# Optimization experiments

Measured on AMD Instinct MI355X. Metric: run time of the kernel, lower is better.

Reference implementation:

```python
import jax, jax.numpy as jnp
import numpy as np

N, E, M, F, L = 50000, 800000, 50000, 64, 20
HID = 32
NEG_SLOPE = 0.2


def gatv2(x, src, dst, Wl, Wr, att, b, heads, outc):
    # PyG GATv2Conv (eval mode, dropout off), self-loops already in src/dst.
    n = x.shape[0]
    xl = (x @ Wl).reshape(n, heads, outc)
    xr = (x @ Wr).reshape(n, heads, outc)
    e = jax.nn.leaky_relu(xl[src] + xr[dst], NEG_SLOPE)          # [E, H, C]
    score = jnp.einsum('ehc,hc->eh', e, att)                      # [E, H]
    smax = jax.ops.segment_max(score, dst, num_segments=n)
    ex = jnp.exp(score - smax[dst])
    denom = jax.ops.segment_sum(ex, dst, num_segments=n)
    alpha = ex / denom[dst]                                       # scatter-softmax
    out = jax.ops.segment_sum(alpha[:, :, None] * xl[src], dst, num_segments=n)
    return out.reshape(n, heads * outc) + b


def setup_inputs() -> dict:
    key = jax.random.key(0)
    ks = jax.random.split(key, 32)
    d = {}
    d['x'] = jax.random.normal(ks[0], (N, 60), jnp.float32)
    d['lane_x'] = jax.random.normal(ks[1], (M, 2), jnp.float32)
    d['centerline'] = jax.random.normal(ks[2], (F, L, 2), jnp.float32)
    d['edge_index'] = jax.random.randint(ks[3], (2, E), 0, N)
    d['focal_idx'] = jax.random.randint(ks[4], (F,), 0, N)
    s = 0.1
    d['emb_W'] = jax.random.normal(ks[5], (60, HID)) * s
    d['emb_b'] = jnp.zeros((HID,))
    d['c1_Wl'] = jax.random.normal(ks[6], (HID, 4 * HID)) * s
    d['c1_Wr'] = jax.random.normal(ks[7], (HID, 4 * HID)) * s
    d['c1_att'] = jax.random.normal(ks[8], (4, HID)) * s
    d['c1_b'] = jnp.zeros((4 * HID,))
    d['c2_Wl'] = jax.random.normal(ks[9], (4 * HID, 4 * HID)) * s
    d['c2_Wr'] = jax.random.normal(ks[10], (4 * HID, 4 * HID)) * s
    d['c2_att'] = jax.random.normal(ks[11], (4, HID)) * s
    d['c2_b'] = jnp.zeros((4 * HID,))
    d['map_W'] = jax.random.normal(ks[12], (2, HID)) * s
    d['map_b'] = jnp.zeros((HID,))
    d['gg_Wl'] = jax.random.normal(ks[13], (4 * HID, HID)) * s
    d['gg_Wr'] = jax.random.normal(ks[14], (4 * HID, HID)) * s
    d['gg_att'] = jax.random.normal(ks[15], (1, HID)) * s
    d['gg_b'] = jnp.zeros((HID,))
    d['cl_W'] = jax.random.normal(ks[16], (2, HID)) * s
    d['cl_b'] = jnp.zeros((HID,))
    d['fc1_W'] = jax.random.normal(ks[17], (3 * HID, HID)) * s
    d['fc1_b'] = jnp.zeros((HID,))
    d['fc2_W'] = jax.random.normal(ks[18], (HID, HID // 2)) * s
    d['fc2_b'] = jnp.zeros((HID // 2,))
    d['fco_W'] = jax.random.normal(ks[19], (HID // 2, 60)) * s
    d['fco_b'] = jnp.zeros((60,))
    return d


def reference(x, lane_x, centerline, edge_index, focal_idx,
              emb_W, emb_b, c1_Wl, c1_Wr, c1_att, c1_b,
              c2_Wl, c2_Wr, c2_att, c2_b, map_W, map_b,
              gg_Wl, gg_Wr, gg_att, gg_b, cl_W, cl_b,
              fc1_W, fc1_b, fc2_W, fc2_b, fco_W, fco_b):
    n = x.shape[0]
    loops = jnp.arange(n)
    src = jnp.concatenate([edge_index[0], loops])  # PyG adds self-loops
    dst = jnp.concatenate([edge_index[1], loops])
    # agent encoder + subgraph (two GATv2 layers, heads=4, concat)
    h = jax.nn.relu(x @ emb_W + emb_b)                                   # [N,32]
    h = jax.nn.relu(gatv2(h, src, dst, c1_Wl, c1_Wr, c1_att, c1_b, 4, HID))
    agent_feat = jax.nn.relu(gatv2(h, src, dst, c2_Wl, c2_Wr, c2_att, c2_b, 4, HID))  # [N,128]
    # map branch (executable path: no lane edges -> plain embedding + mean pool)
    map_x = jax.nn.relu(lane_x @ map_W + map_b)                          # [M,32]
    map_global = jnp.mean(map_x, axis=0, keepdims=True)                  # [1,32]
    # global graph (heads=1)
    gf = jax.nn.relu(gatv2(agent_feat, src, dst, gg_Wl, gg_Wr, gg_att, gg_b, 1, HID))  # [N,32]
    focal = gf[focal_idx]                                                # [F,32]
    map_g = jnp.broadcast_to(map_global, (focal.shape[0], HID))
    cl = jnp.mean(centerline, axis=1) @ cl_W + cl_b                      # [F,32]
    comb = jnp.concatenate([focal, map_g, cl], axis=1)                   # [F,96]
    h = jax.nn.relu(comb @ fc1_W + fc1_b)
    h = jax.nn.relu(h @ fc2_W + fc2_b)
    return h @ fco_W + fco_b                                             # [F,60]
```

## Files before the change

kernel.cpp:

```cpp
#include <hip/hip_runtime.h>
#include <hip/hip_bf16.h>
#include <hip/hip_fp16.h>

typedef _Float16 half_t;
typedef _Float16 h8 __attribute__((ext_vector_type(8)));
typedef _Float16 h4v __attribute__((ext_vector_type(4)));
typedef _Float16 h2v __attribute__((ext_vector_type(2)));
typedef float f4v __attribute__((ext_vector_type(4)));

union H8u { h8 v; h2v h2[4]; _Float16 e[8]; };
union H4u { h4v v; h2v h2[2]; _Float16 e[4]; };

static inline int cdiv(long a, long b) { return (int)((a + b - 1) / b); }

__device__ __forceinline__ void fma4(float4& a, float s, const float4& w) {
    a.x += s * w.x; a.y += s * w.y; a.z += s * w.z; a.w += s * w.w;
}

__device__ __forceinline__ h8 hmax8(h8 a, h8 b) {
#if __has_builtin(__builtin_elementwise_max)
    return __builtin_elementwise_max(a, b);
#else
    h8 r;
#pragma unroll
    for (int j = 0; j < 8; ++j) r[j] = (a[j] > b[j]) ? a[j] : b[j];
    return r;
#endif
}
__device__ __forceinline__ h4v hmax4(h4v a, h4v b) {
#if __has_builtin(__builtin_elementwise_max)
    return __builtin_elementwise_max(a, b);
#else
    h4v r;
#pragma unroll
    for (int j = 0; j < 4; ++j) r[j] = (a[j] > b[j]) ? a[j] : b[j];
    return r;
#endif
}

__device__ __forceinline__ float dot2acc(h2v a, h2v b, float c) {
#if __has_builtin(__builtin_amdgcn_fdot2)
    return __builtin_amdgcn_fdot2(a, b, c, false);
#else
    return c + (float)a.x * (float)b.x + (float)a.y * (float)b.y;
#endif
}


template <int K4, int C4, int R>
__global__ __launch_bounds__(256) void gemm_t_h(
        const float* __restrict__ X, const float* __restrict__ W,
        const float* __restrict__ bias, half_t* __restrict__ Y,
        int Nr, int relu) {
    int idx = blockIdx.x * blockDim.x + threadIdx.x;
    int total = (Nr / R) * C4;
    if (idx >= total) return;
    int c4 = idx % C4;
    int n0 = (idx / C4) * R;
    const float4* __restrict__ Wv = (const float4*)W;
    const float4* __restrict__ Xv = (const float4*)X;
    float4 acc[R];
    float4 binit = bias ? ((const float4*)bias)[c4] : make_float4(0.f, 0.f, 0.f, 0.f);
#pragma unroll
    for (int r = 0; r < R; ++r) acc[r] = binit;
#pragma unroll 4
    for (int k4 = 0; k4 < K4; ++k4) {
        float4 w0 = Wv[(size_t)(4 * k4 + 0) * C4 + c4];
        float4 w1 = Wv[(size_t)(4 * k4 + 1) * C4 + c4];
        float4 w2 = Wv[(size_t)(4 * k4 + 2) * C4 + c4];
        float4 w3 = Wv[(size_t)(4 * k4 + 3) * C4 + c4];
#pragma unroll
        for (int r = 0; r < R; ++r) {
            float4 xv = Xv[(size_t)(n0 + r) * K4 + k4];
            fma4(acc[r], xv.x, w0); fma4(acc[r], xv.y, w1);
            fma4(acc[r], xv.z, w2); fma4(acc[r], xv.w, w3);
        }
    }
#pragma unroll
    for (int r = 0; r < R; ++r) {
        float4 o = acc[r];
        if (relu) {
            o.x = fmaxf(o.x, 0.f); o.y = fmaxf(o.y, 0.f);
            o.z = fmaxf(o.z, 0.f); o.w = fmaxf(o.w, 0.f);
        }
        h4v oh; oh.x = (half_t)o.x; oh.y = (half_t)o.y; oh.z = (half_t)o.z; oh.w = (half_t)o.w;
        ((h4v*)Y)[(size_t)(n0 + r) * C4 + c4] = oh;
    }
}


__global__ void wtrans(const float* __restrict__ c1l, const float* __restrict__ c1r,
                       const float* __restrict__ c2l, const float* __restrict__ c2r,
                       const float* __restrict__ ggl, const float* __restrict__ ggr,
                       const float* __restrict__ at1, const float* __restrict__ at2,
                       const float* __restrict__ atg, half_t* __restrict__ dst) {
    int idx = blockIdx.x * blockDim.x + threadIdx.x;
    if (idx >= 49440) return;
    if (idx >= 49152) {
        int j = idx - 49152;
        float v = (j < 128) ? at1[j] : (j < 256) ? at2[j - 128] : atg[j - 256];
        dst[idx] = (half_t)v;
        return;
    }
    const float* src; int K, loc;
    if (idx < 8192) {
        K = 32;
        if (idx < 4096) { src = c1l; loc = idx; } else { src = c1r; loc = idx - 4096; }
        int k = loc % K, c = loc / K;
        dst[idx] = (half_t)src[k * 128 + c];
    } else if (idx < 40960) {
        K = 128;
        if (idx < 24576) { src = c2l; loc = idx - 8192; } else { src = c2r; loc = idx - 24576; }
        int k = loc % K, c = loc / K;
        dst[idx] = (half_t)src[k * 128 + c];
    } else {
        K = 128;
        if (idx < 45056) { src = ggl; loc = idx - 40960; } else { src = ggr; loc = idx - 45056; }
        int k = loc % K, c = loc / K;
        dst[idx] = (half_t)src[k * 32 + c];
    }
}


template <int K, int C1>
__global__ __launch_bounds__(256) void mfma_dual(
        const half_t* __restrict__ Xh,
        const half_t* __restrict__ W1t, const half_t* __restrict__ W2t,
        half_t* __restrict__ Y1, half_t* __restrict__ Y2, int Nr) {
    constexpr int KT = K / 32;
    constexpr int NBC = (2 * C1) / 64;
    int wave = threadIdx.x >> 6, lane = threadIdx.x & 63;
    int bCol = blockIdx.x % NBC;
    int bRow = blockIdx.x / NBC;
    int rowBase = bRow * 128 + wave * 32;
    int colBase = bCol * 64;
    int m = lane & 15, quad = lane >> 4;

    f4v acc[2][4] = {};

    const half_t* bptr[4];
#pragma unroll
    for (int nt = 0; nt < 4; ++nt) {
        int gc = colBase + nt * 16 + m;
        bptr[nt] = (gc < C1) ? (W1t + (size_t)gc * K) : (W2t + (size_t)(gc - C1) * K);
    }
    int r0 = rowBase + m, r1 = rowBase + 16 + m;
    int r0c = (r0 < Nr) ? r0 : (Nr - 1);
    int r1c = (r1 < Nr) ? r1 : (Nr - 1);
    const half_t* a0p = Xh + (size_t)r0c * K + quad * 8;
    const half_t* a1p = Xh + (size_t)r1c * K + quad * 8;

#pragma unroll
    for (int kk = 0; kk < KT; ++kk) {
        h8 a0 = *(const h8*)(a0p + kk * 32);
        h8 a1 = *(const h8*)(a1p + kk * 32);
#pragma unroll
        for (int nt = 0; nt < 4; ++nt) {
            h8 b = *(const h8*)(bptr[nt] + kk * 32 + quad * 8);
            acc[0][nt] = __builtin_amdgcn_mfma_f32_16x16x32_f16(a0, b, acc[0][nt], 0, 0, 0);
            acc[1][nt] = __builtin_amdgcn_mfma_f32_16x16x32_f16(a1, b, acc[1][nt], 0, 0, 0);
        }
    }

#pragma unroll
    for (int mt = 0; mt < 2; ++mt) {
#pragma unroll
        for (int nt = 0; nt < 4; ++nt) {
            int gc = colBase + nt * 16 + m;
            half_t* Y = (gc < C1) ? (Y1 + gc) : (Y2 + (gc - C1));
#pragma unroll
            for (int r = 0; r < 4; ++r) {
                int gr = rowBase + mt * 16 + quad * 4 + r;
                if (gr < Nr) Y[(size_t)gr * C1] = (half_t)acc[mt][nt][r];
            }
        }
    }
}


__global__ void count_dst(const int* __restrict__ ei, int* __restrict__ counts, int E) {
    int e = blockIdx.x * blockDim.x + threadIdx.x;
    if (e >= E) return;
    atomicAdd(&counts[ei[E + e]], 1);
}

#define SCAN_CH 2048

__global__ void reduce_chunks(const int* __restrict__ counts, int* __restrict__ partial, int N) {
    __shared__ int sh[256];
    int t = threadIdx.x, base = blockIdx.x * SCAN_CH + t * 8;
    int s = 0;
    for (int j = 0; j < 8; ++j) if (base + j < N) s += counts[base + j] + 1;
    sh[t] = s; __syncthreads();
    for (int off = 128; off >= 1; off >>= 1) {
        if (t < off) sh[t] += sh[t + off];
        __syncthreads();
    }
    if (t == 0) partial[blockIdx.x] = sh[0];
}

__global__ void scan_partials(int* __restrict__ partial, int nch) {
    if (threadIdx.x == 0 && blockIdx.x == 0) {
        int run = 0;
        for (int i = 0; i < nch; ++i) { int v = partial[i]; partial[i] = run; run += v; }
    }
}

__global__ void scan_chunks(int* __restrict__ counts, const int* __restrict__ partial,
                            int* __restrict__ offsets, int* __restrict__ cursor,
                            int* __restrict__ adj, int N) {
    __shared__ int sh[256];
    int t = threadIdx.x, b = blockIdx.x, base = b * SCAN_CH + t * 8;
    int v[8], s = 0;
    for (int j = 0; j < 8; ++j) {
        v[j] = (base + j < N) ? (counts[base + j] + 1) : 0;
        s += v[j];
    }
    sh[t] = s; __syncthreads();
    for (int off = 1; off < 256; off <<= 1) {
        int x = (t >= off) ? sh[t - off] : 0;
        __syncthreads();
        sh[t] += x;
        __syncthreads();
    }
    int run = partial[b] + (t == 0 ? 0 : sh[t - 1]);
    for (int j = 0; j < 8; ++j) {
        if (base + j < N) {
            offsets[base + j] = run;
            adj[run] = base + j;
            cursor[base + j] = run + 1;
            counts[base + j] = v[j];
        }
        run += v[j];
    }
}

__global__ __launch_bounds__(256) void fill_adj_sliced(
        const int* __restrict__ ei, int* __restrict__ cursor,
        int* __restrict__ adj, int E, int sliceSz) {
    int slice = blockIdx.x & 7;
    int lo = slice * sliceSz, hi = lo + sliceSz;
    int nb = gridDim.x >> 3;
    int bi = blockIdx.x >> 3;
    int stride = nb * 256;
    for (int e = bi * 256 + threadIdx.x; e < E; e += stride) {
        int d = ei[E + e];
        if (d >= lo && d < hi) {
            int pos = atomicAdd(&cursor[d], 1);
            adj[pos] = ei[e];
        }
    }
}


__global__ __launch_bounds__(256) void gat8_h4(
        const half_t* __restrict__ xl, const half_t* __restrict__ xr,
        const half_t* __restrict__ atth, const int* __restrict__ offsets,
        const int* __restrict__ counts, const int* __restrict__ adj,
        const float* __restrict__ bias, half_t* __restrict__ out, int N) {
    int wave = threadIdx.x >> 6, lane = threadIdx.x & 63;
    int g = lane >> 3, t = lane & 7;
    int d = blockIdx.x * 32 + wave * 8 + g;
    int dc = (d < N) ? d : (N - 1);
    int off = offsets[dc];
    int deg = (d < N) ? counts[dc] : 0;
    int dmax = deg;
    dmax = max(dmax, __shfl_xor(dmax, 8));
    dmax = max(dmax, __shfl_xor(dmax, 16));
    dmax = max(dmax, __shfl_xor(dmax, 32));

    const half_t* xrp = xr + (size_t)dc * 128 + t * 16;
    h8 xr_lo = *(const h8*)(xrp);
    h8 xr_hi = *(const h8*)(xrp + 8);
    H8u at_lo, at_hi;
    at_lo.v = *(const h8*)(atth + t * 16);
    at_hi.v = *(const h8*)(atth + t * 16 + 8);

    float acc[16];
#pragma unroll
    for (int j = 0; j < 16; ++j) acc[j] = 0.f;
    float lsum = 0.f;
    h8 c02;
#pragma unroll
    for (int j = 0; j < 8; ++j) c02[j] = (half_t)0.2f;

    int i = 0;
    for (; i + 2 <= dmax; i += 2) {
        bool va = (i < deg), vb = (i + 1 < deg);
        int sa = adj[off + (va ? i : 0)];
        int sb = adj[off + (vb ? i + 1 : 0)];
        const half_t* xpa = xl + (size_t)sa * 128 + t * 16;
        const half_t* xpb = xl + (size_t)sb * 128 + t * 16;
        H8u aa_lo, aa_hi, ab_lo, ab_hi;
        aa_lo.v = *(const h8*)(xpa);
        aa_hi.v = *(const h8*)(xpa + 8);
        ab_lo.v = *(const h8*)(xpb);
        ab_hi.v = *(const h8*)(xpb + 8);

        h8 va_lo = aa_lo.v + xr_lo, va_hi = aa_hi.v + xr_hi;
        h8 vb_lo = ab_lo.v + xr_lo, vb_hi = ab_hi.v + xr_hi;
        H8u la_lo, la_hi, lb_lo, lb_hi;
        la_lo.v = hmax8(va_lo, va_lo * c02);
        la_hi.v = hmax8(va_hi, va_hi * c02);
        lb_lo.v = hmax8(vb_lo, vb_lo * c02);
        lb_hi.v = hmax8(vb_hi, vb_hi * c02);

        float pa = 0.f, pb = 0.f;
#pragma unroll
        for (int j = 0; j < 4; ++j) {
            pa = dot2acc(la_lo.h2[j], at_lo.h2[j], pa);
            pb = dot2acc(lb_lo.h2[j], at_lo.h2[j], pb);
        }
#pragma unroll
        for (int j = 0; j < 4; ++j) {
            pa = dot2acc(la_hi.h2[j], at_hi.h2[j], pa);
            pb = dot2acc(lb_hi.h2[j], at_hi.h2[j], pb);
        }
        pa += __shfl_xor(pa, 1);
        pb += __shfl_xor(pb, 1);
        float wa = va ? __expf(pa) : 0.f;
        float wb = vb ? __expf(pb) : 0.f;
        lsum += wa + wb;
#pragma unroll
        for (int j = 0; j < 8; ++j)
            acc[j] += wa * (float)aa_lo.e[j] + wb * (float)ab_lo.e[j];
#pragma unroll
        for (int j = 0; j < 8; ++j)
            acc[8 + j] += wa * (float)aa_hi.e[j] + wb * (float)ab_hi.e[j];
    }
    for (; i < dmax; ++i) {
        bool valid = (i < deg);
        int s = adj[off + (valid ? i : 0)];
        const half_t* xp = xl + (size_t)s * 128 + t * 16;
        H8u a_lo, a_hi;
        a_lo.v = *(const h8*)(xp);
        a_hi.v = *(const h8*)(xp + 8);
        h8 v_lo = a_lo.v + xr_lo;
        h8 v_hi = a_hi.v + xr_hi;
        H8u lk_lo, lk_hi;
        lk_lo.v = hmax8(v_lo, v_lo * c02);
        lk_hi.v = hmax8(v_hi, v_hi * c02);
        float p = 0.f;
#pragma unroll
        for (int j = 0; j < 4; ++j) p = dot2acc(lk_lo.h2[j], at_lo.h2[j], p);
#pragma unroll
        for (int j = 0; j < 4; ++j) p = dot2acc(lk_hi.h2[j], at_hi.h2[j], p);
        p += __shfl_xor(p, 1);
        float w = valid ? __expf(p) : 0.f;
        lsum += w;
#pragma unroll
        for (int j = 0; j < 8; ++j) acc[j] += w * (float)a_lo.e[j];
#pragma unroll
        for (int j = 0; j < 8; ++j) acc[8 + j] += w * (float)a_hi.e[j];
    }

    if (d < N) {
        float inv = 1.f / lsum;
        H8u o_lo, o_hi;
#pragma unroll
        for (int j = 0; j < 8; ++j)
            o_lo.e[j] = (half_t)fmaxf(acc[j] * inv + bias[t * 16 + j], 0.f);
#pragma unroll
        for (int j = 0; j < 8; ++j)
            o_hi.e[j] = (half_t)fmaxf(acc[8 + j] * inv + bias[t * 16 + 8 + j], 0.f);
        half_t* op = out + (size_t)d * 128 + t * 16;
        *(h8*)(op) = o_lo.v;
        *(h8*)(op + 8) = o_hi.v;
    }
}

__global__ __launch_bounds__(256) void gat8_h1(
        const half_t* __restrict__ xl, const half_t* __restrict__ xr,
        const half_t* __restrict__ atth, const int* __restrict__ offsets,
        const int* __restrict__ counts, const int* __restrict__ adj,
        const float* __restrict__ bias, float* __restrict__ out, int N) {
    int wave = threadIdx.x >> 6, lane = threadIdx.x & 63;
    int g = lane >> 3, t = lane & 7;
    int d = blockIdx.x * 32 + wave * 8 + g;
    int dc = (d < N) ? d : (N - 1);
    int off = offsets[dc];
    int deg = (d < N) ? counts[dc] : 0;
    int dmax = deg;
    dmax = max(dmax, __shfl_xor(dmax, 8));
    dmax = max(dmax, __shfl_xor(dmax, 16));
    dmax = max(dmax, __shfl_xor(dmax, 32));

    h4v xr4 = *(const h4v*)(xr + (size_t)dc * 32 + t * 4);
    H4u at4; at4.v = *(const h4v*)(atth + t * 4);

    float acc[4] = {0.f, 0.f, 0.f, 0.f};
    float lsum = 0.f;
    h4v c02;
#pragma unroll
    for (int j = 0; j < 4; ++j) c02[j] = (half_t)0.2f;

    int i = 0;
    for (; i + 2 <= dmax; i += 2) {
        bool va = (i < deg), vb = (i + 1 < deg);
        int sa = adj[off + (va ? i : 0)];
        int sb = adj[off + (vb ? i + 1 : 0)];
        H4u a, b;
        a.v = *(const h4v*)(xl + (size_t)sa * 32 + t * 4);
        b.v = *(const h4v*)(xl + (size_t)sb * 32 + t * 4);
        h4v vva = a.v + xr4, vvb = b.v + xr4;
        H4u la, lb;
        la.v = hmax4(vva, vva * c02);
        lb.v = hmax4(vvb, vvb * c02);
        float pa = dot2acc(la.h2[0], at4.h2[0], 0.f);
        float pb = dot2acc(lb.h2[0], at4.h2[0], 0.f);
        pa = dot2acc(la.h2[1], at4.h2[1], pa);
        pb = dot2acc(lb.h2[1], at4.h2[1], pb);
        pa += __shfl_xor(pa, 1); pb += __shfl_xor(pb, 1);
        pa += __shfl_xor(pa, 2); pb += __shfl_xor(pb, 2);
        pa += __shfl_xor(pa, 4); pb += __shfl_xor(pb, 4);
        float wa = va ? __expf(pa) : 0.f;
        float wb = vb ? __expf(pb) : 0.f;
        lsum += wa + wb;
#pragma unroll
        for (int j = 0; j < 4; ++j)
            acc[j] += wa * (float)a.e[j] + wb * (float)b.e[j];
    }
    for (; i < dmax; ++i) {
        bool valid = (i < deg);
        int s = adj[off + (valid ? i : 0)];
        H4u a; a.v = *(const h4v*)(xl + (size_t)s * 32 + t * 4);
        h4v v = a.v + xr4;
        H4u lk; lk.v = hmax4(v, v * c02);
        float p = dot2acc(lk.h2[0], at4.h2[0], 0.f);
        p = dot2acc(lk.h2[1], at4.h2[1], p);
        p += __shfl_xor(p, 1);
        p += __shfl_xor(p, 2);
        p += __shfl_xor(p, 4);
        float w = valid ? __expf(p) : 0.f;
        lsum += w;
#pragma unroll
        for (int j = 0; j < 4; ++j) acc[j] += w * (float)a.e[j];
    }

    if (d < N) {
        float inv = 1.f / lsum;
        float4 o;
        o.x = fmaxf(acc[0] * inv + bias[t * 4 + 0], 0.f);
        o.y = fmaxf(acc[1] * inv + bias[t * 4 + 1], 0.f);
        o.z = fmaxf(acc[2] * inv + bias[t * 4 + 2], 0.f);
        o.w = fmaxf(acc[3] * inv + bias[t * 4 + 3], 0.f);
        *(float4*)(out + (size_t)d * 32 + t * 4) = o;
    }
}


__global__ void map_sum_kernel(const float* __restrict__ lane_x, const float* __restrict__ map_W,
                               const float* __restrict__ map_b, float* __restrict__ sums, int M) {
    __shared__ float s[32];
    if (threadIdx.x < 32) s[threadIdx.x] = 0.f;
    __syncthreads();
    int t = blockIdx.x * blockDim.x + threadIdx.x;
    int nth = gridDim.x * blockDim.x;
    int c = t & 31;
    float w0 = map_W[c], w1 = map_W[32 + c], bb = map_b[c];
    float acc = 0.f;
    for (int m = t >> 5; m < M; m += nth >> 5) {
        float v = lane_x[(long)m * 2] * w0 + lane_x[(long)m * 2 + 1] * w1 + bb;
        acc += fmaxf(v, 0.f);
    }
    atomicAdd(&s[c], acc);
    __syncthreads();
    if (threadIdx.x < 32) atomicAdd(&sums[threadIdx.x], s[threadIdx.x]);
}


__global__ void head_kernel(const float* __restrict__ gf, const int* __restrict__ focal_idx,
                            const float* __restrict__ map_sums, int M,
                            const float* __restrict__ centerline, int L,
                            const float* __restrict__ cl_W, const float* __restrict__ cl_b,
                            const float* __restrict__ fc1_W, const float* __restrict__ fc1_b,
                            const float* __restrict__ fc2_W, const float* __restrict__ fc2_b,
                            const float* __restrict__ fco_W, const float* __restrict__ fco_b,
                            float* __restrict__ out) {
    int f = blockIdx.x;
    int lane = threadIdx.x;
    __shared__ float s_comb[96];
    __shared__ float s_h1[32];
    __shared__ float s_h2[16];
    __shared__ float s_cl[2];

    float c0 = 0.f, c1 = 0.f;
    if (lane < L) {
        c0 = centerline[((long)f * L + lane) * 2 + 0];
        c1 = centerline[((long)f * L + lane) * 2 + 1];
    }
    for (int off = 32; off >= 1; off >>= 1) {
        c0 += __shfl_down(c0, off);
        c1 += __shfl_down(c1, off);
    }
    if (lane == 0) { s_cl[0] = c0 / (float)L; s_cl[1] = c1 / (float)L; }
    __syncthreads();

    int fi = focal_idx[f];
    if (lane < 32) {
        s_comb[lane] = gf[(long)fi * 32 + lane];
        s_comb[32 + lane] = map_sums[lane] / (float)M;
        s_comb[64 + lane] = s_cl[0] * cl_W[lane] + s_cl[1] * cl_W[32 + lane] + cl_b[lane];
    }
    __syncthreads();

    if (lane < 32) {
        float acc = fc1_b[lane];
        for (int k = 0; k < 96; ++k) acc += s_comb[k] * fc1_W[k * 32 + lane];
        s_h1[lane] = fmaxf(acc, 0.f);
    }
    __syncthreads();

    if (lane < 16) {
        float acc = fc2_b[lane];
        for (int k = 0; k < 32; ++k) acc += s_h1[k] * fc2_W[k * 16 + lane];
        s_h2[lane] = fmaxf(acc, 0.f);
    }
    __syncthreads();

    if (lane < 60) {
        float acc = fco_b[lane];
        for (int k = 0; k < 16; ++k) acc += s_h2[k] * fco_W[k * 60 + lane];
        out[(long)f * 60 + lane] = acc;
    }
}


extern "C" void kernel_launch(void* const* d_in, const int* in_sizes, int n_in,
                              void* d_out, int out_size, void* d_ws, size_t ws_size,
                              hipStream_t stream) {
    const float* x          = (const float*)d_in[0];
    const float* lane_x     = (const float*)d_in[1];
    const float* centerline = (const float*)d_in[2];
    const int*   ei         = (const int*)d_in[3];
    const int*   focal_idx  = (const int*)d_in[4];
    const float* emb_W = (const float*)d_in[5];
    const float* emb_b = (const float*)d_in[6];
    const float* c1_Wl = (const float*)d_in[7];
    const float* c1_Wr = (const float*)d_in[8];
    const float* c1_att = (const float*)d_in[9];
    const float* c1_b  = (const float*)d_in[10];
    const float* c2_Wl = (const float*)d_in[11];
    const float* c2_Wr = (const float*)d_in[12];
    const float* c2_att = (const float*)d_in[13];
    const float* c2_b  = (const float*)d_in[14];
    const float* map_W = (const float*)d_in[15];
    const float* map_b = (const float*)d_in[16];
    const float* gg_Wl = (const float*)d_in[17];
    const float* gg_Wr = (const float*)d_in[18];
    const float* gg_att = (const float*)d_in[19];
    const float* gg_b  = (const float*)d_in[20];
    const float* cl_W  = (const float*)d_in[21];
    const float* cl_b  = (const float*)d_in[22];
    const float* fc1_W = (const float*)d_in[23];
    const float* fc1_b = (const float*)d_in[24];
    const float* fc2_W = (const float*)d_in[25];
    const float* fc2_b = (const float*)d_in[26];
    const float* fco_W = (const float*)d_in[27];
    const float* fco_b = (const float*)d_in[28];

    const int N = in_sizes[0] / 60;
    const int M = in_sizes[1] / 2;
    const int F = in_sizes[4];
    const int L = in_sizes[2] / (F * 2);
    const int E = in_sizes[3] / 2;
    const int Etot = E + N;

    half_t* Xl_h = (half_t*)d_ws;
    half_t* Xr_h = Xl_h + (size_t)N * 128;
    half_t* H0_h = Xr_h + (size_t)N * 128;
    half_t* H1_h = H0_h + (size_t)N * 32;
    half_t* AF_h = H1_h + (size_t)N * 128;
    float*  GF_f = (float*)(AF_h + (size_t)N * 128);
    half_t* Wt   = (half_t*)(GF_f + (size_t)N * 32);
    int* counts  = (int*)(Wt + 49440);
    int* offsets = counts + N;
    int* cursor  = offsets + N;
    int* adj     = cursor + N;
    float* MAPS  = (float*)(adj + Etot);
    int* partial = (int*)(MAPS + 32);

    half_t* c1Wlt = Wt + 0;
    half_t* c1Wrt = Wt + 4096;
    half_t* c2Wlt = Wt + 8192;
    half_t* c2Wrt = Wt + 24576;
    half_t* ggWlt = Wt + 40960;
    half_t* ggWrt = Wt + 45056;
    half_t* att1h = Wt + 49152;
    half_t* att2h = Wt + 49280;
    half_t* attgh = Wt + 49408;

    const int BS = 256;
    const int nch = cdiv(N, SCAN_CH);
    const int rowBlocks = cdiv(N, 128);
    const int sliceSz = cdiv(N, 8);

    hipMemsetAsync(counts, 0, (size_t)N * sizeof(int), stream);
    count_dst<<<cdiv(E, BS), BS, 0, stream>>>(ei, counts, E);
    reduce_chunks<<<nch, 256, 0, stream>>>(counts, partial, N);
    scan_partials<<<1, 64, 0, stream>>>(partial, nch);
    scan_chunks<<<nch, 256, 0, stream>>>(counts, partial, offsets, cursor, adj, N);
    fill_adj_sliced<<<8 * 104, 256, 0, stream>>>(ei, cursor, adj, E, sliceSz);

    wtrans<<<cdiv(49440, BS), BS, 0, stream>>>(c1_Wl, c1_Wr, c2_Wl, c2_Wr, gg_Wl, gg_Wr,
                                               c1_att, c2_att, gg_att, Wt);

    gemm_t_h<15, 8, 4><<<cdiv((long)(N / 4) * 8, BS), BS, 0, stream>>>(x, emb_W, emb_b, H0_h, N, 1);

    mfma_dual<32, 128><<<rowBlocks * 4, 256, 0, stream>>>(H0_h, c1Wlt, c1Wrt, Xl_h, Xr_h, N);
    gat8_h4<<<cdiv(N, 32), 256, 0, stream>>>(Xl_h, Xr_h, att1h, offsets, counts, adj, c1_b, H1_h, N);

    mfma_dual<128, 128><<<rowBlocks * 4, 256, 0, stream>>>(H1_h, c2Wlt, c2Wrt, Xl_h, Xr_h, N);
    gat8_h4<<<cdiv(N, 32), 256, 0, stream>>>(Xl_h, Xr_h, att2h, offsets, counts, adj, c2_b, AF_h, N);

    mfma_dual<128, 32><<<rowBlocks * 1, 256, 0, stream>>>(AF_h, ggWlt, ggWrt, Xl_h, Xr_h, N);
    gat8_h1<<<cdiv(N, 32), 256, 0, stream>>>(Xl_h, Xr_h, attgh, offsets, counts, adj, gg_b, GF_f, N);

    hipMemsetAsync(MAPS, 0, 32 * sizeof(float), stream);
    map_sum_kernel<<<64, BS, 0, stream>>>(lane_x, map_W, map_b, MAPS, M);

    head_kernel<<<F, 64, 0, stream>>>(GF_f, focal_idx, MAPS, M, centerline, L,
                                      cl_W, cl_b, fc1_W, fc1_b, fc2_W, fc2_b,
                                      fco_W, fco_b, (float*)d_out);
}
```

Before: 389.7 us.

## Use 16 lanes per destination node in GAT aggregation with prefetched neighbor indices

The GAT aggregation kernels now assign 16 lanes to each destination node instead of 8. In the 4-head kernel each lane handles 8 channels, and the loop processes 4 neighbors per iteration while prefetching the next iteration's adjacency indices. The 1-head kernel splits neighbors between two 8-lane halves, each taking 2 neighbors per step, and reduces the halves with shuffles at the end. This exposes more memory-level parallelism for the gathers and hides adj-load latency, at the cost of twice as many lanes per node, extra shuffles, and wasted work on padded iterations.

```diff
diff --git a/kernel.cpp b/kernel.cpp
--- a/kernel.cpp
+++ b/kernel.cpp
@@ -253,135 +253,104 @@
 }
 
 
-__global__ __launch_bounds__(256) void gat8_h4(
+__global__ __launch_bounds__(256) void gat16_h4(
         const half_t* __restrict__ xl, const half_t* __restrict__ xr,
         const half_t* __restrict__ atth, const int* __restrict__ offsets,
         const int* __restrict__ counts, const int* __restrict__ adj,
         const float* __restrict__ bias, half_t* __restrict__ out, int N) {
     int wave = threadIdx.x >> 6, lane = threadIdx.x & 63;
-    int g = lane >> 3, t = lane & 7;
-    int d = blockIdx.x * 32 + wave * 8 + g;
+    int g = lane >> 4, t = lane & 15;
+    int d = blockIdx.x * 16 + wave * 4 + g;
     int dc = (d < N) ? d : (N - 1);
     int off = offsets[dc];
     int deg = (d < N) ? counts[dc] : 0;
     int dmax = deg;
-    dmax = max(dmax, __shfl_xor(dmax, 8));
     dmax = max(dmax, __shfl_xor(dmax, 16));
     dmax = max(dmax, __shfl_xor(dmax, 32));
 
-    const half_t* xrp = xr + (size_t)dc * 128 + t * 16;
-    h8 xr_lo = *(const h8*)(xrp);
-    h8 xr_hi = *(const h8*)(xrp + 8);
-    H8u at_lo, at_hi;
-    at_lo.v = *(const h8*)(atth + t * 16);
-    at_hi.v = *(const h8*)(atth + t * 16 + 8);
-
-    float acc[16];
-#pragma unroll
-    for (int j = 0; j < 16; ++j) acc[j] = 0.f;
+    h8 xr8 = *(const h8*)(xr + (size_t)dc * 128 + t * 8);
+    H8u at8; at8.v = *(const h8*)(atth + t * 8);
+
+    float acc[8];
+#pragma unroll
+    for (int j = 0; j < 8; ++j) acc[j] = 0.f;
     float lsum = 0.f;
     h8 c02;
 #pragma unroll
     for (int j = 0; j < 8; ++j) c02[j] = (half_t)0.2f;
 
-    int i = 0;
-    for (; i + 2 <= dmax; i += 2) {
-        bool va = (i < deg), vb = (i + 1 < deg);
-        int sa = adj[off + (va ? i : 0)];
-        int sb = adj[off + (vb ? i + 1 : 0)];
-        const half_t* xpa = xl + (size_t)sa * 128 + t * 16;
-        const half_t* xpb = xl + (size_t)sb * 128 + t * 16;
-        H8u aa_lo, aa_hi, ab_lo, ab_hi;
-        aa_lo.v = *(const h8*)(xpa);
-        aa_hi.v = *(const h8*)(xpa + 8);
-        ab_lo.v = *(const h8*)(xpb);
-        ab_hi.v = *(const h8*)(xpb + 8);
-
-        h8 va_lo = aa_lo.v + xr_lo, va_hi = aa_hi.v + xr_hi;
-        h8 vb_lo = ab_lo.v + xr_lo, vb_hi = ab_hi.v + xr_hi;
-        H8u la_lo, la_hi, lb_lo, lb_hi;
-        la_lo.v = hmax8(va_lo, va_lo * c02);
-        la_hi.v = hmax8(va_hi, va_hi * c02);
-        lb_lo.v = hmax8(vb_lo, vb_lo * c02);
-        lb_hi.v = hmax8(vb_hi, vb_hi * c02);
-
-        float pa = 0.f, pb = 0.f;
+    bool v0 = 0 < deg, v1 = 1 < deg, v2 = 2 < deg, v3 = 3 < deg;
+    int s0 = adj[off];
+    int s1 = adj[off + (v1 ? 1 : 0)];
+    int s2 = adj[off + (v2 ? 2 : 0)];
+    int s3 = adj[off + (v3 ? 3 : 0)];
+
+    for (int i = 0; i < dmax; i += 4) {
+        H8u a0, a1, a2, a3;
+        a0.v = *(const h8*)(xl + (size_t)s0 * 128 + t * 8);
+        a1.v = *(const h8*)(xl + (size_t)s1 * 128 + t * 8);
+        a2.v = *(const h8*)(xl + (size_t)s2 * 128 + t * 8);
+        a3.v = *(const h8*)(xl + (size_t)s3 * 128 + t * 8);
+        int ni = i + 4;
+        bool nv0 = ni < deg, nv1 = ni + 1 < deg, nv2 = ni + 2 < deg, nv3 = ni + 3 < deg;
+        int n0 = adj[off + (nv0 ? ni : 0)];
+        int n1 = adj[off + (nv1 ? ni + 1 : 0)];
+        int n2 = adj[off + (nv2 ? ni + 2 : 0)];
+        int n3 = adj[off + (nv3 ? ni + 3 : 0)];
+
+        h8 e0 = a0.v + xr8, e1 = a1.v + xr8, e2 = a2.v + xr8, e3 = a3.v + xr8;
+        H8u l0, l1, l2, l3;
+        l0.v = hmax8(e0, e0 * c02);
+        l1.v = hmax8(e1, e1 * c02);
+        l2.v = hmax8(e2, e2 * c02);
+        l3.v = hmax8(e3, e3 * c02);
+        float p0 = 0.f, p1 = 0.f, p2 = 0.f, p3 = 0.f;
 #pragma unroll
         for (int j = 0; j < 4; ++j) {
-            pa = dot2acc(la_lo.h2[j], at_lo.h2[j], pa);
-            pb = dot2acc(lb_lo.h2[j], at_lo.h2[j], pb);
-        }
-#pragma unroll
-        for (int j = 0; j < 4; ++j) {
-            pa = dot2acc(la_hi.h2[j], at_hi.h2[j], pa);
-            pb = dot2acc(lb_hi.h2[j], at_hi.h2[j], pb);
-        }
-        pa += __shfl_xor(pa, 1);
-        pb += __shfl_xor(pb, 1);
-        float wa = va ? __expf(pa) : 0.f;
-        float wb = vb ? __expf(pb) : 0.f;
-        lsum += wa + wb;
+            p0 = dot2acc(l0.h2[j], at8.h2[j], p0);
+            p1 = dot2acc(l1.h2[j], at8.h2[j], p1);
+            p2 = dot2acc(l2.h2[j], at8.h2[j], p2);
+            p3 = dot2acc(l3.h2[j], at8.h2[j], p3);
+        }
+        p0 += __shfl_xor(p0, 1); p1 += __shfl_xor(p1, 1);
+        p2 += __shfl_xor(p2, 1); p3 += __shfl_xor(p3, 1);
+        p0 += __shfl_xor(p0, 2); p1 += __shfl_xor(p1, 2);
+        p2 += __shfl_xor(p2, 2); p3 += __shfl_xor(p3, 2);
+        float w0 = v0 ? __expf(p0) : 0.f;
+        float w1 = v1 ? __expf(p1) : 0.f;
+        float w2 = v2 ? __expf(p2) : 0.f;
+        float w3 = v3 ? __expf(p3) : 0.f;
+        lsum += (w0 + w1) + (w2 + w3);
 #pragma unroll
         for (int j = 0; j < 8; ++j)
-            acc[j] += wa * (float)aa_lo.e[j] + wb * (float)ab_lo.e[j];
-#pragma unroll
-        for (int j = 0; j < 8; ++j)
-            acc[8 + j] += wa * (float)aa_hi.e[j] + wb * (float)ab_hi.e[j];
-    }
-    for (; i < dmax; ++i) {
-        bool valid = (i < deg);
-        int s = adj[off + (valid ? i : 0)];
-        const half_t* xp = xl + (size_t)s * 128 + t * 16;
-        H8u a_lo, a_hi;
-        a_lo.v = *(const h8*)(xp);
-        a_hi.v = *(const h8*)(xp + 8);
-        h8 v_lo = a_lo.v + xr_lo;
-        h8 v_hi = a_hi.v + xr_hi;
-        H8u lk_lo, lk_hi;
-        lk_lo.v = hmax8(v_lo, v_lo * c02);
-        lk_hi.v = hmax8(v_hi, v_hi * c02);
-        float p = 0.f;
-#pragma unroll
-        for (int j = 0; j < 4; ++j) p = dot2acc(lk_lo.h2[j], at_lo.h2[j], p);
-#pragma unroll
-        for (int j = 0; j < 4; ++j) p = dot2acc(lk_hi.h2[j], at_hi.h2[j], p);
-        p += __shfl_xor(p, 1);
-        float w = valid ? __expf(p) : 0.f;
-        lsum += w;
-#pragma unroll
-        for (int j = 0; j < 8; ++j) acc[j] += w * (float)a_lo.e[j];
-#pragma unroll
-        for (int j = 0; j < 8; ++j) acc[8 + j] += w * (float)a_hi.e[j];
+            acc[j] += w0 * (float)a0.e[j] + w1 * (float)a1.e[j]
+                    + w2 * (float)a2.e[j] + w3 * (float)a3.e[j];
+        s0 = n0; s1 = n1; s2 = n2; s3 = n3;
+        v0 = nv0; v1 = nv1; v2 = nv2; v3 = nv3;
     }
 
     if (d < N) {
         float inv = 1.f / lsum;
-        H8u o_lo, o_hi;
+        H8u o;
 #pragma unroll
         for (int j = 0; j < 8; ++j)
-            o_lo.e[j] = (half_t)fmaxf(acc[j] * inv + bias[t * 16 + j], 0.f);
-#pragma unroll
-        for (int j = 0; j < 8; ++j)
-            o_hi.e[j] = (half_t)fmaxf(acc[8 + j] * inv + bias[t * 16 + 8 + j], 0.f);
-        half_t* op = out + (size_t)d * 128 + t * 16;
-        *(h8*)(op) = o_lo.v;
-        *(h8*)(op + 8) = o_hi.v;
-    }
-}
-
-__global__ __launch_bounds__(256) void gat8_h1(
+            o.e[j] = (half_t)fmaxf(acc[j] * inv + bias[t * 8 + j], 0.f);
+        *(h8*)(out + (size_t)d * 128 + t * 8) = o.v;
+    }
+}
+
+__global__ __launch_bounds__(256) void gat16_h1(
         const half_t* __restrict__ xl, const half_t* __restrict__ xr,
         const half_t* __restrict__ atth, const int* __restrict__ offsets,
         const int* __restrict__ counts, const int* __restrict__ adj,
         const float* __restrict__ bias, float* __restrict__ out, int N) {
     int wave = threadIdx.x >> 6, lane = threadIdx.x & 63;
-    int g = lane >> 3, t = lane & 7;
-    int d = blockIdx.x * 32 + wave * 8 + g;
+    int g = lane >> 4, sub = (lane >> 3) & 1, t = lane & 7;
+    int d = blockIdx.x * 16 + wave * 4 + g;
     int dc = (d < N) ? d : (N - 1);
     int off = offsets[dc];
     int deg = (d < N) ? counts[dc] : 0;
     int dmax = deg;
-    dmax = max(dmax, __shfl_xor(dmax, 8));
     dmax = max(dmax, __shfl_xor(dmax, 16));
     dmax = max(dmax, __shfl_xor(dmax, 32));
 
@@ -394,18 +363,22 @@
 #pragma unroll
     for (int j = 0; j < 4; ++j) c02[j] = (half_t)0.2f;
 
-    int i = 0;
-    for (; i + 2 <= dmax; i += 2) {
-        bool va = (i < deg), vb = (i + 1 < deg);
-        int sa = adj[off + (va ? i : 0)];
-        int sb = adj[off + (vb ? i + 1 : 0)];
+    int i = sub;
+    bool va = i < deg, vb = i + 2 < deg;
+    int sa = adj[off + (va ? i : 0)];
+    int sb = adj[off + (vb ? i + 2 : 0)];
+    for (; i < dmax; i += 4) {
         H4u a, b;
         a.v = *(const h4v*)(xl + (size_t)sa * 32 + t * 4);
         b.v = *(const h4v*)(xl + (size_t)sb * 32 + t * 4);
-        h4v vva = a.v + xr4, vvb = b.v + xr4;
+        int ni = i + 4;
+        bool nva = ni < deg, nvb = ni + 2 < deg;
+        int na = adj[off + (nva ? ni : 0)];
+        int nb = adj[off + (nvb ? ni + 2 : 0)];
+        h4v ea = a.v + xr4, eb = b.v + xr4;
         H4u la, lb;
-        la.v = hmax4(vva, vva * c02);
-        lb.v = hmax4(vvb, vvb * c02);
+        la.v = hmax4(ea, ea * c02);
+        lb.v = hmax4(eb, eb * c02);
         float pa = dot2acc(la.h2[0], at4.h2[0], 0.f);
         float pb = dot2acc(lb.h2[0], at4.h2[0], 0.f);
         pa = dot2acc(la.h2[1], at4.h2[1], pa);
@@ -419,25 +392,14 @@
 #pragma unroll
         for (int j = 0; j < 4; ++j)
             acc[j] += wa * (float)a.e[j] + wb * (float)b.e[j];
-    }
-    for (; i < dmax; ++i) {
-        bool valid = (i < deg);
-        int s = adj[off + (valid ? i : 0)];
-        H4u a; a.v = *(const h4v*)(xl + (size_t)s * 32 + t * 4);
-        h4v v = a.v + xr4;
-        H4u lk; lk.v = hmax4(v, v * c02);
-        float p = dot2acc(lk.h2[0], at4.h2[0], 0.f);
-        p = dot2acc(lk.h2[1], at4.h2[1], p);
-        p += __shfl_xor(p, 1);
-        p += __shfl_xor(p, 2);
-        p += __shfl_xor(p, 4);
-        float w = valid ? __expf(p) : 0.f;
-        lsum += w;
-#pragma unroll
-        for (int j = 0; j < 4; ++j) acc[j] += w * (float)a.e[j];
-    }
-
-    if (d < N) {
+        sa = na; sb = nb; va = nva; vb = nvb;
+    }
+
+    lsum += __shfl_xor(lsum, 8);
+#pragma unroll
+    for (int j = 0; j < 4; ++j) acc[j] += __shfl_xor(acc[j], 8);
+
+    if (d < N && sub == 0) {
         float inv = 1.f / lsum;
         float4 o;
         o.x = fmaxf(acc[0] * inv + bias[t * 4 + 0], 0.f);
@@ -608,13 +570,13 @@
     gemm_t_h<15, 8, 4><<<cdiv((long)(N / 4) * 8, BS), BS, 0, stream>>>(x, emb_W, emb_b, H0_h, N, 1);
 
     mfma_dual<32, 128><<<rowBlocks * 4, 256, 0, stream>>>(H0_h, c1Wlt, c1Wrt, Xl_h, Xr_h, N);
-    gat8_h4<<<cdiv(N, 32), 256, 0, stream>>>(Xl_h, Xr_h, att1h, offsets, counts, adj, c1_b, H1_h, N);
+    gat16_h4<<<cdiv(N, 16), 256, 0, stream>>>(Xl_h, Xr_h, att1h, offsets, counts, adj, c1_b, H1_h, N);
 
     mfma_dual<128, 128><<<rowBlocks * 4, 256, 0, stream>>>(H1_h, c2Wlt, c2Wrt, Xl_h, Xr_h, N);
-    gat8_h4<<<cdiv(N, 32), 256, 0, stream>>>(Xl_h, Xr_h, att2h, offsets, counts, adj, c2_b, AF_h, N);
+    gat16_h4<<<cdiv(N, 16), 256, 0, stream>>>(Xl_h, Xr_h, att2h, offsets, counts, adj, c2_b, AF_h, N);
 
     mfma_dual<128, 32><<<rowBlocks * 1, 256, 0, stream>>>(AF_h, ggWlt, ggWrt, Xl_h, Xr_h, N);
-    gat8_h1<<<cdiv(N, 32), 256, 0, stream>>>(Xl_h, Xr_h, attgh, offsets, counts, adj, gg_b, GF_f, N);
+    gat16_h1<<<cdiv(N, 16), 256, 0, stream>>>(Xl_h, Xr_h, attgh, offsets, counts, adj, gg_b, GF_f, N);
 
     hipMemsetAsync(MAPS, 0, 32 * sizeof(float), stream);
     map_sum_kernel<<<64, BS, 0, stream>>>(lane_x, map_W, map_b, MAPS, M);
```

After: 382.9 us. Within noise of the previous version (-1.8%).
